# Kernel optimization log

Measured on AMD Instinct MI355X. Metric: run time of the kernel, lower is better.

## Reference

```python
import jax, jax.numpy as jnp
import numpy as np

DIM = 512
HEADS = 8
DIM_HEAD = 64
DIM_INNER = HEADS * DIM_HEAD
NULL_KV = 2
CD_ITERS = 50
CD_K = 8.0
CD_EPS = 0.1
LN_EPS = 1e-5


def setup_inputs() -> dict:
    key = jax.random.key(0)
    k0, k1, k2, k3 = jax.random.split(key, 4)
    b, n = 1, 1024
    x = jax.random.normal(k0, (b, n, DIM), dtype=jnp.float32)
    w_qkv = jax.random.normal(k1, (DIM, 3 * DIM_INNER), dtype=jnp.float32) * (DIM ** -0.5)
    w_out = jax.random.normal(k2, (DIM_INNER, DIM), dtype=jnp.float32) * (DIM_INNER ** -0.5)
    null_kv = jax.random.normal(k3, (2, HEADS, NULL_KV, DIM_HEAD), dtype=jnp.float32)
    ln_g = jnp.ones((DIM,), dtype=jnp.float32)
    ln_b = jnp.zeros((DIM,), dtype=jnp.float32)
    return {"x": x, "w_qkv": w_qkv, "w_out": w_out, "null_kv": null_kv,
            "ln_g": ln_g, "ln_b": ln_b}


def _coor_descent(s, mask, k, n_iters, eps):
    # s: (b, h, i, j); mask True = attend. eps_decay==1 upstream => eps fixed.
    mask_value = -jnp.finfo(s.dtype).max
    logk = jnp.log(jnp.asarray(k, dtype=s.dtype))
    s = jnp.where(mask, s, mask_value)

    def step(carry, _):
        a, b = carry
        sb = jnp.where(mask, (s + b) / eps, mask_value)
        a = eps * (logk - jax.nn.logsumexp(sb, axis=-1, keepdims=True))
        b = -jax.nn.relu(-s - a)
        return (a, b), None

    a0 = jnp.zeros(s.shape[:-1] + (1,), dtype=s.dtype)
    b0 = -s
    (a, b), _ = jax.lax.scan(jax.checkpoint(step), (a0, b0), None, length=n_iters)
    scores = jnp.exp((s + a + b) / eps)
    return jnp.where(mask, scores, 0.0)


def reference(x, w_qkv, w_out, null_kv, ln_g, ln_b):
    b, n, _ = x.shape
    # LayerNorm (biased variance, torch default eps)
    mu = jnp.mean(x, axis=-1, keepdims=True)
    var = jnp.var(x, axis=-1, keepdims=True)
    xn = (x - mu) / jnp.sqrt(var + LN_EPS) * ln_g + ln_b

    qkv = xn @ w_qkv                                  # (b, n, 3*dim_inner)
    q, k, v = jnp.split(qkv, 3, axis=-1)
    to_heads = lambda t: t.reshape(b, n, HEADS, DIM_HEAD).transpose(0, 2, 1, 3)
    q, k, v = to_heads(q), to_heads(k), to_heads(v)   # (b, h, n, d)

    nk = jnp.broadcast_to(null_kv[0], (b, HEADS, NULL_KV, DIM_HEAD))
    nv = jnp.broadcast_to(null_kv[1], (b, HEADS, NULL_KV, DIM_HEAD))
    k = jnp.concatenate([nk, k], axis=-2)             # (b, h, n+nkv, d)
    v = jnp.concatenate([nv, v], axis=-2)

    q = q * (DIM_HEAD ** -0.5)
    sim = jnp.einsum('bhid,bhjd->bhij', q, k)         # (b, h, i, j)
    i, j = sim.shape[-2:]
    causal = jnp.triu(jnp.ones((i, j), dtype=bool), j - i + 1)
    mask = ~causal                                    # True = attend (null kv always visible)

    attn = _coor_descent(sim, mask, CD_K, CD_ITERS, CD_EPS)
    out = jnp.einsum('bhij,bhjd->bhid', attn, v)
    out = out.transpose(0, 2, 1, 3).reshape(b, n, DIM_INNER)
    return out @ w_out
```

## Files before the change

### kernel.cpp

```cpp
#include <hip/hip_runtime.h>
#include <math.h>

#define NHEAD 8
#define SROW 1088
#define PBF  2176
#define VSTR 1056
#define LOGK 2.0794415416798357f

typedef __bf16 bf16x8 __attribute__((ext_vector_type(8)));
typedef __bf16 bf16x4 __attribute__((ext_vector_type(4)));
typedef float  f32x4  __attribute__((ext_vector_type(4)));

__device__ __forceinline__ void split2(float v, __bf16& hi, __bf16& lo) {
    hi = (__bf16)v; lo = (__bf16)(v - (float)hi);
}

__device__ __forceinline__ float dpp_sum64(float x) {
    int v;
    v = __builtin_amdgcn_update_dpp(0, __float_as_int(x), 0x111, 0xf, 0xf, true); x += __int_as_float(v);
    v = __builtin_amdgcn_update_dpp(0, __float_as_int(x), 0x112, 0xf, 0xf, true); x += __int_as_float(v);
    v = __builtin_amdgcn_update_dpp(0, __float_as_int(x), 0x114, 0xf, 0xf, true); x += __int_as_float(v);
    v = __builtin_amdgcn_update_dpp(0, __float_as_int(x), 0x118, 0xf, 0xf, true); x += __int_as_float(v);
    v = __builtin_amdgcn_update_dpp(0, __float_as_int(x), 0x142, 0xa, 0xf, true); x += __int_as_float(v);
    v = __builtin_amdgcn_update_dpp(0, __float_as_int(x), 0x143, 0xc, 0xf, true); x += __int_as_float(v);
    return __int_as_float(__builtin_amdgcn_readlane(__float_as_int(x), 63));
}
__device__ __forceinline__ float dpp_max64(float x) {
    int v;
    v = __builtin_amdgcn_update_dpp(__float_as_int(x), __float_as_int(x), 0x111, 0xf, 0xf, false); x = fmaxf(x, __int_as_float(v));
    v = __builtin_amdgcn_update_dpp(__float_as_int(x), __float_as_int(x), 0x112, 0xf, 0xf, false); x = fmaxf(x, __int_as_float(v));
    v = __builtin_amdgcn_update_dpp(__float_as_int(x), __float_as_int(x), 0x114, 0xf, 0xf, false); x = fmaxf(x, __int_as_float(v));
    v = __builtin_amdgcn_update_dpp(__float_as_int(x), __float_as_int(x), 0x118, 0xf, 0xf, false); x = fmaxf(x, __int_as_float(v));
    v = __builtin_amdgcn_update_dpp(__float_as_int(x), __float_as_int(x), 0x142, 0xa, 0xf, false); x = fmaxf(x, __int_as_float(v));
    v = __builtin_amdgcn_update_dpp(__float_as_int(x), __float_as_int(x), 0x143, 0xc, 0xf, false); x = fmaxf(x, __int_as_float(v));
    return __int_as_float(__builtin_amdgcn_readlane(__float_as_int(x), 63));
}

__global__ __launch_bounds__(128) void ln_split(const float* __restrict__ x,
                                                const float* __restrict__ g,
                                                const float* __restrict__ bb,
                                                __bf16* __restrict__ xnh,
                                                __bf16* __restrict__ xnl) {
    int row = blockIdx.x, tid = threadIdx.x;
    float4 v = ((const float4*)(x + row * 512))[tid];
    float s  = v.x + v.y + v.z + v.w;
    float ss = fmaf(v.x, v.x, fmaf(v.y, v.y, fmaf(v.z, v.z, v.w * v.w)));
#pragma unroll
    for (int off = 32; off; off >>= 1) {
        s  += __shfl_down(s, off);
        ss += __shfl_down(ss, off);
    }
    __shared__ float sm[4];
    if ((tid & 63) == 0) { sm[(tid >> 6) * 2] = s; sm[(tid >> 6) * 2 + 1] = ss; }
    __syncthreads();
    s = sm[0] + sm[2]; ss = sm[1] + sm[3];
    float mu   = s * (1.f / 512);
    float var  = ss * (1.f / 512) - mu * mu;
    float rstd = 1.f / sqrtf(var + 1e-5f);
    float4 gv = ((const float4*)g)[tid];
    float4 bv = ((const float4*)bb)[tid];
    float o[4];
    o[0] = (v.x - mu) * rstd * gv.x + bv.x;
    o[1] = (v.y - mu) * rstd * gv.y + bv.y;
    o[2] = (v.z - mu) * rstd * gv.z + bv.z;
    o[3] = (v.w - mu) * rstd * gv.w + bv.w;
    bf16x4 h4, l4;
#pragma unroll
    for (int e = 0; e < 4; ++e) { __bf16 hi, lo; split2(o[e], hi, lo); h4[e] = hi; l4[e] = lo; }
    *(bf16x4*)(xnh + (size_t)row * 512 + tid * 4) = h4;
    *(bf16x4*)(xnl + (size_t)row * 512 + tid * 4) = l4;
}

__global__ __launch_bounds__(256) void wsplit_qkv(const float* __restrict__ B,
                                                  __bf16* __restrict__ bh,
                                                  __bf16* __restrict__ bl) {
    __shared__ float T[64][65];
    int k0 = blockIdx.x * 64, n0 = blockIdx.y * 64, tid = threadIdx.x;
    int r = tid >> 2, c0 = (tid & 3) << 4;
#pragma unroll
    for (int u = 0; u < 4; ++u) {
        float4 w = *(const float4*)(B + (size_t)(k0 + r) * 1536 + n0 + c0 + 4 * u);
        T[r][c0 + 4 * u + 0] = w.x; T[r][c0 + 4 * u + 1] = w.y;
        T[r][c0 + 4 * u + 2] = w.z; T[r][c0 + 4 * u + 3] = w.w;
    }
    __syncthreads();
    int nr = tid >> 2, kc0 = (tid & 3) << 4;
#pragma unroll
    for (int u = 0; u < 4; ++u) {
        bf16x4 h4, l4;
#pragma unroll
        for (int e = 0; e < 4; ++e) {
            __bf16 hi, lo; split2(T[kc0 + 4 * u + e][nr], hi, lo);
            h4[e] = hi; l4[e] = lo;
        }
        *(bf16x4*)(bh + (size_t)(n0 + nr) * 512 + k0 + kc0 + 4 * u) = h4;
        *(bf16x4*)(bl + (size_t)(n0 + nr) * 512 + k0 + kc0 + 4 * u) = l4;
    }
}

__global__ __launch_bounds__(256) void wsplit_out(const float* __restrict__ B,
                                                  __bf16* __restrict__ wo) {
    __shared__ float T[64][65];
    int k0 = blockIdx.x * 64, n0 = blockIdx.y * 64, tid = threadIdx.x;
    int r = tid >> 2, c0 = (tid & 3) << 4;
#pragma unroll
    for (int u = 0; u < 4; ++u) {
        float4 w = *(const float4*)(B + (size_t)(k0 + r) * 512 + n0 + c0 + 4 * u);
        T[r][c0 + 4 * u + 0] = w.x; T[r][c0 + 4 * u + 1] = w.y;
        T[r][c0 + 4 * u + 2] = w.z; T[r][c0 + 4 * u + 3] = w.w;
    }
    __syncthreads();
    int nr = tid >> 2, kc0 = (tid & 3) << 4;
#pragma unroll
    for (int u = 0; u < 4; ++u) {
        bf16x4 h4;
#pragma unroll
        for (int e = 0; e < 4; ++e) h4[e] = (__bf16)T[kc0 + 4 * u + e][nr];
        *(bf16x4*)(wo + (size_t)(n0 + nr) * 512 + k0 + kc0 + 4 * u) = h4;
    }
}

__global__ __launch_bounds__(256) void nullkv2(const float* __restrict__ nkv,
                                               __bf16* __restrict__ kh,
                                               __bf16* __restrict__ kl,
                                               __bf16* __restrict__ vT) {
    int tid = blockIdx.x * 256 + threadIdx.x;
    int d = tid & 63, p = (tid >> 6) & 1, h = tid >> 7;
    float kvf = nkv[((0 * NHEAD + h) * 2 + p) * 64 + d];
    __bf16 hi, lo; split2(kvf, hi, lo);
    kh[((size_t)h * SROW + p) * 64 + d] = hi;
    kl[((size_t)h * SROW + p) * 64 + d] = lo;
    float vf = nkv[((NHEAD + h) * 2 + p) * 64 + d];
    vT[((size_t)(h * 64) + d) * VSTR + p] = (__bf16)vf;
    int base = tid * 15;
#pragma unroll
    for (int e = 0; e < 15; ++e) {
        int z = base + e;
        int jj = 1026 + (z % 30);
        int hd = z / 30;
        vT[(size_t)hd * VSTR + jj] = (__bf16)0.f;
    }
}

__global__ __launch_bounds__(256, 2) void qkv_mfma(const __bf16* __restrict__ xh,
                                                   const __bf16* __restrict__ xl,
                                                   const __bf16* __restrict__ bh,
                                                   const __bf16* __restrict__ bl,
                                                   __bf16* __restrict__ qh,
                                                   __bf16* __restrict__ ql,
                                                   __bf16* __restrict__ kh,
                                                   __bf16* __restrict__ kl,
                                                   __bf16* __restrict__ vT) {
    int tid = threadIdx.x, l = tid & 63, w = tid >> 6;
    int m0 = blockIdx.x * 32, n0 = blockIdx.y * 64;
    int ms = (w & 1) << 4, nh2 = (w >> 1) << 5;
    int arow = m0 + ms + (l & 15);
    f32x4 acc[2] = {};
    for (int ks = 0; ks < 16; ++ks) {
        int koff = ((l >> 4) << 3) + (ks << 5);
        bf16x8 ah = *(const bf16x8*)(xh + (size_t)arow * 512 + koff);
        bf16x8 al = *(const bf16x8*)(xl + (size_t)arow * 512 + koff);
#pragma unroll
        for (int ct = 0; ct < 2; ++ct) {
            int ncol = n0 + nh2 + (ct << 4) + (l & 15);
            bf16x8 bhv = *(const bf16x8*)(bh + (size_t)ncol * 512 + koff);
            bf16x8 blv = *(const bf16x8*)(bl + (size_t)ncol * 512 + koff);
            acc[ct] = __builtin_amdgcn_mfma_f32_16x16x32_bf16(ah, bhv, acc[ct], 0, 0, 0);
            acc[ct] = __builtin_amdgcn_mfma_f32_16x16x32_bf16(al, bhv, acc[ct], 0, 0, 0);
            acc[ct] = __builtin_amdgcn_mfma_f32_16x16x32_bf16(ah, blv, acc[ct], 0, 0, 0);
        }
    }
#pragma unroll
    for (int ct = 0; ct < 2; ++ct) {
        int c = n0 + nh2 + (ct << 4) + (l & 15);
#pragma unroll
        for (int r = 0; r < 4; ++r) {
            int m = m0 + ms + ((l >> 4) << 2) + r;
            float val = acc[ct][r];
            if (c < 512) {
                int h = c >> 6, d = c & 63;
                __bf16 hi, lo; split2(val * 1.25f, hi, lo);
                qh[(((size_t)(h << 10)) + m) * 64 + d] = hi;
                ql[(((size_t)(h << 10)) + m) * 64 + d] = lo;
            } else if (c < 1024) {
                int c2 = c - 512, h = c2 >> 6, d = c2 & 63;
                __bf16 hi, lo; split2(val, hi, lo);
                kh[((size_t)h * SROW + 2 + m) * 64 + d] = hi;
                kl[((size_t)h * SROW + 2 + m) * 64 + d] = lo;
            } else {
                int c2 = c - 1024, h = c2 >> 6, d = c2 & 63;
                vT[((size_t)(h * 64) + d) * VSTR + 2 + m] = (__bf16)val;
            }
        }
    }
}

__global__ __launch_bounds__(256, 2) void qk_mfma(const __bf16* __restrict__ qh,
                                                  const __bf16* __restrict__ ql,
                                                  const __bf16* __restrict__ kh,
                                                  const __bf16* __restrict__ kl,
                                                  float* __restrict__ s) {
    int b = blockIdx.x, h = blockIdx.y;
    int ti = (int)((-3.0f + sqrtf(9.0f + 8.0f * (float)b)) * 0.5f);
    while ((ti + 1) * (ti + 4) / 2 <= b) ++ti;
    while (ti * (ti + 3) / 2 > b) --ti;
    int tj = b - ti * (ti + 3) / 2;
    int i0 = ti << 6, j0 = tj << 6;

    int tid = threadIdx.x, l = tid & 63, w = tid >> 6;
    int arow = i0 + (w << 4) + (l & 15);
    const __bf16* qhb = qh + ((size_t)(h << 10) + arow) * 64;
    const __bf16* qlb = ql + ((size_t)(h << 10) + arow) * 64;
    f32x4 acc[4] = {};
#pragma unroll
    for (int ks = 0; ks < 2; ++ks) {
        int koff = ((l >> 4) << 3) + (ks << 5);
        bf16x8 ah = *(const bf16x8*)(qhb + koff);
        bf16x8 al = *(const bf16x8*)(qlb + koff);
#pragma unroll
        for (int ct = 0; ct < 4; ++ct) {
            int j = j0 + (ct << 4) + (l & 15);
            bf16x8 bhv = *(const bf16x8*)(kh + ((size_t)h * SROW + j) * 64 + koff);
            bf16x8 blv = *(const bf16x8*)(kl + ((size_t)h * SROW + j) * 64 + koff);
            acc[ct] = __builtin_amdgcn_mfma_f32_16x16x32_bf16(ah, bhv, acc[ct], 0, 0, 0);
            acc[ct] = __builtin_amdgcn_mfma_f32_16x16x32_bf16(al, bhv, acc[ct], 0, 0, 0);
            acc[ct] = __builtin_amdgcn_mfma_f32_16x16x32_bf16(ah, blv, acc[ct], 0, 0, 0);
        }
    }
#pragma unroll
    for (int ct = 0; ct < 4; ++ct) {
        int j = j0 + (ct << 4) + (l & 15);
#pragma unroll
        for (int r = 0; r < 4; ++r) {
            int i = i0 + (w << 4) + ((l >> 4) << 2) + r;
            s[((size_t)(h << 10) + i) * SROW + j] = acc[ct][r];
        }
    }
}

__global__ __launch_bounds__(64, 4) void cd_kernel(float* __restrict__ s) {
    int lane = threadIdx.x, p = blockIdx.x;
    int h = p >> 9, ip = p & 511;
    int iA = 1023 - ip, iB = ip;
    int nvA = iA + 3, nvB = iB + 3;
    float* rA = s + ((size_t)(h << 10) + iA) * SROW;
    float* rB = s + ((size_t)(h << 10) + iB) * SROW;
    int jb = lane << 2;

    float4 sA[5], sB[3];
#pragma unroll
    for (int t = 0; t < 5; ++t) {
        if (jb + (t << 8) < SROW) sA[t] = *(const float4*)(rA + jb + (t << 8));
        else { sA[t].x = sA[t].y = sA[t].z = sA[t].w = -INFINITY; }
    }
#pragma unroll
    for (int t = 0; t < 3; ++t) sB[t] = *(const float4*)(rB + jb + (t << 8));

    float mA = -INFINITY, mB = -INFINITY;
#pragma unroll
    for (int t = 0; t < 5; ++t) {
        float* sp = (float*)&sA[t];
#pragma unroll
        for (int c = 0; c < 4; ++c) {
            int j = jb + c + (t << 8);
            float v = (j < nvA) ? sp[c] : -INFINITY;
            sp[c] = v; mA = fmaxf(mA, v);
        }
    }
#pragma unroll
    for (int t = 0; t < 3; ++t) {
        float* sp = (float*)&sB[t];
#pragma unroll
        for (int c = 0; c < 4; ++c) {
            int j = jb + c + (t << 8);
            float v = (j < nvB) ? sp[c] : -INFINITY;
            sp[c] = v; mB = fmaxf(mB, v);
        }
    }
    mA = dpp_max64(mA); mB = dpp_max64(mB);

    float4 EA[5], E2A[5], EB[3], E2B[3];
#pragma unroll
    for (int t = 0; t < 5; ++t) {
        float* sp = (float*)&sA[t]; float* ep = (float*)&EA[t]; float* e2p = (float*)&E2A[t];
#pragma unroll
        for (int c = 0; c < 4; ++c) { float e = __expf(sp[c] - mA); ep[c] = e; e2p[c] = e * e; }
    }
#pragma unroll
    for (int t = 0; t < 3; ++t) {
        float* sp = (float*)&sB[t]; float* ep = (float*)&EB[t]; float* e2p = (float*)&E2B[t];
#pragma unroll
        for (int c = 0; c < 4; ++c) { float e = __expf(sp[c] - mB); ep[c] = e; e2p[c] = e * e; }
    }

    float gA = LOGK - __logf((float)nvA) + mA;
    float gB = LOGK - __logf((float)nvB) + mB;
    bool dA = false, dB = false;
#pragma unroll 1
    for (int it = 1; it < 50; ++it) {
        if (!dA) {
            float eg = __expf(fminf(gA, 80.f));
            float a0 = 0.f, a1 = 0.f, a2 = 0.f, a3 = 0.f;
#pragma unroll
            for (int t = 0; t < 5; ++t) {
                a0 += fminf(((float*)&EA[t])[0], ((float*)&E2A[t])[0] * eg);
                a1 += fminf(((float*)&EA[t])[1], ((float*)&E2A[t])[1] * eg);
                a2 += fminf(((float*)&EA[t])[2], ((float*)&E2A[t])[2] * eg);
                a3 += fminf(((float*)&EA[t])[3], ((float*)&E2A[t])[3] * eg);
            }
            float sum = dpp_sum64((a0 + a1) + (a2 + a3));
            float g2 = LOGK - __logf(sum);
            dA = (__float_as_int(g2) == __float_as_int(gA));
            gA = g2;
        }
        if (!dB) {
            float eg = __expf(fminf(gB, 80.f));
            float b0 = 0.f, b1 = 0.f, b2 = 0.f, b3 = 0.f;
#pragma unroll
            for (int t = 0; t < 3; ++t) {
                b0 += fminf(((float*)&EB[t])[0], ((float*)&E2B[t])[0] * eg);
                b1 += fminf(((float*)&EB[t])[1], ((float*)&E2B[t])[1] * eg);
                b2 += fminf(((float*)&EB[t])[2], ((float*)&E2B[t])[2] * eg);
                b3 += fminf(((float*)&EB[t])[3], ((float*)&E2B[t])[3] * eg);
            }
            float sum = dpp_sum64((b0 + b1) + (b2 + b3));
            float g2 = LOGK - __logf(sum);
            dB = (__float_as_int(g2) == __float_as_int(gB));
            gB = g2;
        }
        if (dA && dB) break;
    }

    float egA = __expf(fminf(gA, 80.f));
    float egB = __expf(fminf(gB, 80.f));
    __bf16* pA = (__bf16*)rA;
    __bf16* pB = (__bf16*)rB;
#pragma unroll
    for (int t = 0; t < 5; ++t) {
        if (jb + (t << 8) < SROW) {
            bf16x4 pv;
#pragma unroll
            for (int c = 0; c < 4; ++c) {
                float wv = ((float*)&EA[t])[c] * egA;
                pv[c] = (__bf16)(wv * fminf(1.f, wv));
            }
            *(bf16x4*)(pA + jb + (t << 8)) = pv;
        }
    }
#pragma unroll
    for (int t = 0; t < 3; ++t) {
        bf16x4 pv;
#pragma unroll
        for (int c = 0; c < 4; ++c) {
            float wv = ((float*)&EB[t])[c] * egB;
            pv[c] = (__bf16)(wv * fminf(1.f, wv));
        }
        *(bf16x4*)(pB + jb + (t << 8)) = pv;
    }
    bf16x4 z4 = {};
#pragma unroll
    for (int t = 3; t < 5; ++t) {
        if (jb + (t << 8) < SROW) *(bf16x4*)(pB + jb + (t << 8)) = z4;
    }
}

__global__ __launch_bounds__(256, 2) void pv_mfma(const float* __restrict__ s,
                                                  const __bf16* __restrict__ vT,
                                                  __bf16* __restrict__ ao) {
    int i0 = blockIdx.x << 4, h = blockIdx.y;
    int tid = threadIdx.x, l = tid & 63, w = tid >> 6;
    const __bf16* pbase = (const __bf16*)s;
    int arow = i0 + (l & 15);
    int dcol = (w << 4) + (l & 15);
    const __bf16* pr = pbase + ((size_t)(h << 10) + arow) * PBF;
    const __bf16* vr = vT + ((size_t)(h << 6) + dcol) * VSTR;
    f32x4 acc0 = {}, acc1 = {};
    int kb = (l >> 4) << 3;
#pragma unroll 4
    for (int ks = 0; ks < 32; ks += 2) {
        bf16x8 a0 = *(const bf16x8*)(pr + kb + (ks << 5));
        bf16x8 b0 = *(const bf16x8*)(vr + kb + (ks << 5));
        bf16x8 a1 = *(const bf16x8*)(pr + kb + ((ks + 1) << 5));
        bf16x8 b1 = *(const bf16x8*)(vr + kb + ((ks + 1) << 5));
        acc0 = __builtin_amdgcn_mfma_f32_16x16x32_bf16(a0, b0, acc0, 0, 0, 0);
        acc1 = __builtin_amdgcn_mfma_f32_16x16x32_bf16(a1, b1, acc1, 0, 0, 0);
    }
    {
        bf16x8 a0 = *(const bf16x8*)(pr + kb + (32 << 5));
        bf16x8 b0 = *(const bf16x8*)(vr + kb + (32 << 5));
        acc0 = __builtin_amdgcn_mfma_f32_16x16x32_bf16(a0, b0, acc0, 0, 0, 0);
    }
#pragma unroll
    for (int r = 0; r < 4; ++r) {
        int i = i0 + ((l >> 4) << 2) + r;
        ao[(size_t)i * 512 + (h << 6) + dcol] = (__bf16)(acc0[r] + acc1[r]);
    }
}

__global__ __launch_bounds__(256, 2) void out_mfma(const __bf16* __restrict__ ao,
                                                   const __bf16* __restrict__ wo,
                                                   float* __restrict__ out) {
    int m0 = blockIdx.x << 4, bn = blockIdx.y;
    int tid = threadIdx.x, l = tid & 63, w = tid >> 6;
    int arow = m0 + (l & 15);
    int ncol = (bn << 6) + (w << 4) + (l & 15);
    const __bf16* ar = ao + (size_t)arow * 512;
    const __bf16* br = wo + (size_t)ncol * 512;
    f32x4 acc0 = {}, acc1 = {};
    int kb = (l >> 4) << 3;
#pragma unroll 4
    for (int ks = 0; ks < 16; ks += 2) {
        bf16x8 a0 = *(const bf16x8*)(ar + kb + (ks << 5));
        bf16x8 b0 = *(const bf16x8*)(br + kb + (ks << 5));
        bf16x8 a1 = *(const bf16x8*)(ar + kb + ((ks + 1) << 5));
        bf16x8 b1 = *(const bf16x8*)(br + kb + ((ks + 1) << 5));
        acc0 = __builtin_amdgcn_mfma_f32_16x16x32_bf16(a0, b0, acc0, 0, 0, 0);
        acc1 = __builtin_amdgcn_mfma_f32_16x16x32_bf16(a1, b1, acc1, 0, 0, 0);
    }
#pragma unroll
    for (int r = 0; r < 4; ++r) {
        int m = m0 + ((l >> 4) << 2) + r;
        out[(size_t)m * 512 + ncol] = acc0[r] + acc1[r];
    }
}

extern "C" void kernel_launch(void* const* d_in, const int* in_sizes, int n_in,
                              void* d_out, int out_size, void* d_ws, size_t ws_size,
                              hipStream_t stream) {
    const float* x      = (const float*)d_in[0];
    const float* w_qkv  = (const float*)d_in[1];
    const float* w_out  = (const float*)d_in[2];
    const float* nullkv = (const float*)d_in[3];
    const float* ln_g   = (const float*)d_in[4];
    const float* ln_b   = (const float*)d_in[5];
    float* ws = (float*)d_ws;
    float* out = (float*)d_out;

    float* base = ws;
    __bf16* xnh = (__bf16*)(base);              base += 262144;
    __bf16* xnl = (__bf16*)(base);              base += 262144;
    __bf16* wqh = (__bf16*)(base);              base += 393216;
    __bf16* wql = (__bf16*)(base);              base += 393216;
    __bf16* qh  = (__bf16*)(base);              base += 262144;
    __bf16* ql  = (__bf16*)(base);              base += 262144;
    __bf16* kh  = (__bf16*)(base);              base += 278528;
    __bf16* kl  = (__bf16*)(base);              base += 278528;
    __bf16* vT  = (__bf16*)(base);              base += 270336;
    __bf16* wo  = (__bf16*)(base);              base += 131072;
    __bf16* ao  = (__bf16*)(base);              base += 262144;
    float*  s   = base;

    hipLaunchKernelGGL(ln_split,   dim3(1024),    dim3(128), 0, stream, x, ln_g, ln_b, xnh, xnl);
    hipLaunchKernelGGL(wsplit_qkv, dim3(8, 24),   dim3(256), 0, stream, w_qkv, wqh, wql);
    hipLaunchKernelGGL(wsplit_out, dim3(8, 8),    dim3(256), 0, stream, w_out, wo);
    hipLaunchKernelGGL(nullkv2,    dim3(4),       dim3(256), 0, stream, nullkv, kh, kl, vT);
    hipLaunchKernelGGL(qkv_mfma,   dim3(32, 24),  dim3(256), 0, stream, xnh, xnl, wqh, wql, qh, ql, kh, kl, vT);
    hipLaunchKernelGGL(qk_mfma,    dim3(152, 8),  dim3(256), 0, stream, qh, ql, kh, kl, s);
    hipLaunchKernelGGL(cd_kernel,  dim3(4096),    dim3(64),  0, stream, s);
    hipLaunchKernelGGL(pv_mfma,    dim3(64, 8),   dim3(256), 0, stream, s, vT, ao);
    hipLaunchKernelGGL(out_mfma,   dim3(64, 8),   dim3(256), 0, stream, ao, wo, out);
}
```

Baseline: 180.7 us.

## Fuse prep kernels into one launch and slim coordinate-descent register footprint

Merges the layernorm split, both weight split/transposes and the null-kv setup into a single prep kernel dispatched by block index, replacing four launches with one. The coordinate-descent kernel stops keeping a separate squared-exponential array and computes e*min(1,e*eg) on the fly, which cuts register use so the launch bounds can target two waves per block and higher occupancy. This costs an extra multiply per element in the inner loop and adds branch divergence between block roles in the prep kernel.

```diff
diff --git a/kernel.cpp b/kernel.cpp
--- a/kernel.cpp
+++ b/kernel.cpp
@@ -36,109 +36,113 @@
     return __int_as_float(__builtin_amdgcn_readlane(__float_as_int(x), 63));
 }
 
-__global__ __launch_bounds__(128) void ln_split(const float* __restrict__ x,
-                                                const float* __restrict__ g,
-                                                const float* __restrict__ bb,
-                                                __bf16* __restrict__ xnh,
-                                                __bf16* __restrict__ xnl) {
-    int row = blockIdx.x, tid = threadIdx.x;
-    float4 v = ((const float4*)(x + row * 512))[tid];
-    float s  = v.x + v.y + v.z + v.w;
-    float ss = fmaf(v.x, v.x, fmaf(v.y, v.y, fmaf(v.z, v.z, v.w * v.w)));
-#pragma unroll
-    for (int off = 32; off; off >>= 1) {
-        s  += __shfl_down(s, off);
-        ss += __shfl_down(ss, off);
-    }
-    __shared__ float sm[4];
-    if ((tid & 63) == 0) { sm[(tid >> 6) * 2] = s; sm[(tid >> 6) * 2 + 1] = ss; }
-    __syncthreads();
-    s = sm[0] + sm[2]; ss = sm[1] + sm[3];
-    float mu   = s * (1.f / 512);
-    float var  = ss * (1.f / 512) - mu * mu;
-    float rstd = 1.f / sqrtf(var + 1e-5f);
-    float4 gv = ((const float4*)g)[tid];
-    float4 bv = ((const float4*)bb)[tid];
-    float o[4];
-    o[0] = (v.x - mu) * rstd * gv.x + bv.x;
-    o[1] = (v.y - mu) * rstd * gv.y + bv.y;
-    o[2] = (v.z - mu) * rstd * gv.z + bv.z;
-    o[3] = (v.w - mu) * rstd * gv.w + bv.w;
-    bf16x4 h4, l4;
-#pragma unroll
-    for (int e = 0; e < 4; ++e) { __bf16 hi, lo; split2(o[e], hi, lo); h4[e] = hi; l4[e] = lo; }
-    *(bf16x4*)(xnh + (size_t)row * 512 + tid * 4) = h4;
-    *(bf16x4*)(xnl + (size_t)row * 512 + tid * 4) = l4;
-}
-
-__global__ __launch_bounds__(256) void wsplit_qkv(const float* __restrict__ B,
-                                                  __bf16* __restrict__ bh,
-                                                  __bf16* __restrict__ bl) {
+__global__ __launch_bounds__(256) void prep_kernel(const float* __restrict__ x,
+                                                   const float* __restrict__ g,
+                                                   const float* __restrict__ bb,
+                                                   const float* __restrict__ w_qkv,
+                                                   const float* __restrict__ w_out,
+                                                   const float* __restrict__ nkv,
+                                                   __bf16* __restrict__ xnh,
+                                                   __bf16* __restrict__ xnl,
+                                                   __bf16* __restrict__ wqh,
+                                                   __bf16* __restrict__ wql,
+                                                   __bf16* __restrict__ wo,
+                                                   __bf16* __restrict__ kh,
+                                                   __bf16* __restrict__ kl,
+                                                   __bf16* __restrict__ vT) {
     __shared__ float T[64][65];
-    int k0 = blockIdx.x * 64, n0 = blockIdx.y * 64, tid = threadIdx.x;
-    int r = tid >> 2, c0 = (tid & 3) << 4;
-#pragma unroll
-    for (int u = 0; u < 4; ++u) {
-        float4 w = *(const float4*)(B + (size_t)(k0 + r) * 1536 + n0 + c0 + 4 * u);
-        T[r][c0 + 4 * u + 0] = w.x; T[r][c0 + 4 * u + 1] = w.y;
-        T[r][c0 + 4 * u + 2] = w.z; T[r][c0 + 4 * u + 3] = w.w;
-    }
-    __syncthreads();
-    int nr = tid >> 2, kc0 = (tid & 3) << 4;
-#pragma unroll
-    for (int u = 0; u < 4; ++u) {
+    __shared__ float sm[2][4];
+    int b = blockIdx.x, tid = threadIdx.x;
+
+    if (b < 512) {
+        int half = tid >> 7, t = tid & 127;
+        int row = (b << 1) + half;
+        float4 v = ((const float4*)(x + (size_t)row * 512))[t];
+        float s  = v.x + v.y + v.z + v.w;
+        float ss = fmaf(v.x, v.x, fmaf(v.y, v.y, fmaf(v.z, v.z, v.w * v.w)));
+#pragma unroll
+        for (int off = 32; off; off >>= 1) {
+            s  += __shfl_down(s, off);
+            ss += __shfl_down(ss, off);
+        }
+        int wih = (tid >> 6) & 1;
+        if ((tid & 63) == 0) { sm[half][wih * 2] = s; sm[half][wih * 2 + 1] = ss; }
+        __syncthreads();
+        s = sm[half][0] + sm[half][2]; ss = sm[half][1] + sm[half][3];
+        float mu   = s * (1.f / 512);
+        float var  = ss * (1.f / 512) - mu * mu;
+        float rstd = 1.f / sqrtf(var + 1e-5f);
+        float4 gv = ((const float4*)g)[t];
+        float4 bv = ((const float4*)bb)[t];
+        float o[4];
+        o[0] = (v.x - mu) * rstd * gv.x + bv.x;
+        o[1] = (v.y - mu) * rstd * gv.y + bv.y;
+        o[2] = (v.z - mu) * rstd * gv.z + bv.z;
+        o[3] = (v.w - mu) * rstd * gv.w + bv.w;
         bf16x4 h4, l4;
 #pragma unroll
-        for (int e = 0; e < 4; ++e) {
-            __bf16 hi, lo; split2(T[kc0 + 4 * u + e][nr], hi, lo);
-            h4[e] = hi; l4[e] = lo;
-        }
-        *(bf16x4*)(bh + (size_t)(n0 + nr) * 512 + k0 + kc0 + 4 * u) = h4;
-        *(bf16x4*)(bl + (size_t)(n0 + nr) * 512 + k0 + kc0 + 4 * u) = l4;
-    }
-}
-
-__global__ __launch_bounds__(256) void wsplit_out(const float* __restrict__ B,
-                                                  __bf16* __restrict__ wo) {
-    __shared__ float T[64][65];
-    int k0 = blockIdx.x * 64, n0 = blockIdx.y * 64, tid = threadIdx.x;
-    int r = tid >> 2, c0 = (tid & 3) << 4;
-#pragma unroll
-    for (int u = 0; u < 4; ++u) {
-        float4 w = *(const float4*)(B + (size_t)(k0 + r) * 512 + n0 + c0 + 4 * u);
-        T[r][c0 + 4 * u + 0] = w.x; T[r][c0 + 4 * u + 1] = w.y;
-        T[r][c0 + 4 * u + 2] = w.z; T[r][c0 + 4 * u + 3] = w.w;
-    }
-    __syncthreads();
-    int nr = tid >> 2, kc0 = (tid & 3) << 4;
-#pragma unroll
-    for (int u = 0; u < 4; ++u) {
-        bf16x4 h4;
-#pragma unroll
-        for (int e = 0; e < 4; ++e) h4[e] = (__bf16)T[kc0 + 4 * u + e][nr];
-        *(bf16x4*)(wo + (size_t)(n0 + nr) * 512 + k0 + kc0 + 4 * u) = h4;
-    }
-}
-
-__global__ __launch_bounds__(256) void nullkv2(const float* __restrict__ nkv,
-                                               __bf16* __restrict__ kh,
-                                               __bf16* __restrict__ kl,
-                                               __bf16* __restrict__ vT) {
-    int tid = blockIdx.x * 256 + threadIdx.x;
-    int d = tid & 63, p = (tid >> 6) & 1, h = tid >> 7;
-    float kvf = nkv[((0 * NHEAD + h) * 2 + p) * 64 + d];
-    __bf16 hi, lo; split2(kvf, hi, lo);
-    kh[((size_t)h * SROW + p) * 64 + d] = hi;
-    kl[((size_t)h * SROW + p) * 64 + d] = lo;
-    float vf = nkv[((NHEAD + h) * 2 + p) * 64 + d];
-    vT[((size_t)(h * 64) + d) * VSTR + p] = (__bf16)vf;
-    int base = tid * 15;
-#pragma unroll
-    for (int e = 0; e < 15; ++e) {
-        int z = base + e;
-        int jj = 1026 + (z % 30);
-        int hd = z / 30;
-        vT[(size_t)hd * VSTR + jj] = (__bf16)0.f;
+        for (int e = 0; e < 4; ++e) { __bf16 hi, lo; split2(o[e], hi, lo); h4[e] = hi; l4[e] = lo; }
+        *(bf16x4*)(xnh + (size_t)row * 512 + t * 4) = h4;
+        *(bf16x4*)(xnl + (size_t)row * 512 + t * 4) = l4;
+    } else if (b < 704) {
+        int b2 = b - 512;
+        int k0 = (b2 & 7) * 64, n0 = (b2 >> 3) * 64;
+        int r = tid >> 2, c0 = (tid & 3) << 4;
+#pragma unroll
+        for (int u = 0; u < 4; ++u) {
+            float4 w = *(const float4*)(w_qkv + (size_t)(k0 + r) * 1536 + n0 + c0 + 4 * u);
+            T[r][c0 + 4 * u + 0] = w.x; T[r][c0 + 4 * u + 1] = w.y;
+            T[r][c0 + 4 * u + 2] = w.z; T[r][c0 + 4 * u + 3] = w.w;
+        }
+        __syncthreads();
+        int nr = tid >> 2, kc0 = (tid & 3) << 4;
+#pragma unroll
+        for (int u = 0; u < 4; ++u) {
+            bf16x4 h4, l4;
+#pragma unroll
+            for (int e = 0; e < 4; ++e) {
+                __bf16 hi, lo; split2(T[kc0 + 4 * u + e][nr], hi, lo);
+                h4[e] = hi; l4[e] = lo;
+            }
+            *(bf16x4*)(wqh + (size_t)(n0 + nr) * 512 + k0 + kc0 + 4 * u) = h4;
+            *(bf16x4*)(wql + (size_t)(n0 + nr) * 512 + k0 + kc0 + 4 * u) = l4;
+        }
+    } else if (b < 768) {
+        int b2 = b - 704;
+        int k0 = (b2 & 7) * 64, n0 = (b2 >> 3) * 64;
+        int r = tid >> 2, c0 = (tid & 3) << 4;
+#pragma unroll
+        for (int u = 0; u < 4; ++u) {
+            float4 w = *(const float4*)(w_out + (size_t)(k0 + r) * 512 + n0 + c0 + 4 * u);
+            T[r][c0 + 4 * u + 0] = w.x; T[r][c0 + 4 * u + 1] = w.y;
+            T[r][c0 + 4 * u + 2] = w.z; T[r][c0 + 4 * u + 3] = w.w;
+        }
+        __syncthreads();
+        int nr = tid >> 2, kc0 = (tid & 3) << 4;
+#pragma unroll
+        for (int u = 0; u < 4; ++u) {
+            bf16x4 h4;
+#pragma unroll
+            for (int e = 0; e < 4; ++e) h4[e] = (__bf16)T[kc0 + 4 * u + e][nr];
+            *(bf16x4*)(wo + (size_t)(n0 + nr) * 512 + k0 + kc0 + 4 * u) = h4;
+        }
+    } else {
+        int t2 = (b - 768) * 256 + tid;
+        int d = t2 & 63, p = (t2 >> 6) & 1, h = t2 >> 7;
+        float kvf = nkv[((0 * NHEAD + h) * 2 + p) * 64 + d];
+        __bf16 hi, lo; split2(kvf, hi, lo);
+        kh[((size_t)h * SROW + p) * 64 + d] = hi;
+        kl[((size_t)h * SROW + p) * 64 + d] = lo;
+        float vf = nkv[((NHEAD + h) * 2 + p) * 64 + d];
+        vT[((size_t)(h * 64) + d) * VSTR + p] = (__bf16)vf;
+        int base = t2 * 15;
+#pragma unroll
+        for (int e = 0; e < 15; ++e) {
+            int z = base + e;
+            int jj = 1026 + (z % 30);
+            int hd = z / 30;
+            vT[(size_t)hd * VSTR + jj] = (__bf16)0.f;
+        }
     }
 }
 
@@ -238,8 +242,9 @@
     }
 }
 
-__global__ __launch_bounds__(64, 4) void cd_kernel(float* __restrict__ s) {
-    int lane = threadIdx.x, p = blockIdx.x;
+__global__ __launch_bounds__(128, 8) void cd_kernel(float* __restrict__ s) {
+    int lane = threadIdx.x & 63;
+    int p = (blockIdx.x << 1) + (threadIdx.x >> 6);
     int h = p >> 9, ip = p & 511;
     int iA = 1023 - ip, iB = ip;
     int nvA = iA + 3, nvB = iB + 3;
@@ -247,19 +252,19 @@
     float* rB = s + ((size_t)(h << 10) + iB) * SROW;
     int jb = lane << 2;
 
-    float4 sA[5], sB[3];
+    float4 EA[5], EB[3];
 #pragma unroll
     for (int t = 0; t < 5; ++t) {
-        if (jb + (t << 8) < SROW) sA[t] = *(const float4*)(rA + jb + (t << 8));
-        else { sA[t].x = sA[t].y = sA[t].z = sA[t].w = -INFINITY; }
-    }
-#pragma unroll
-    for (int t = 0; t < 3; ++t) sB[t] = *(const float4*)(rB + jb + (t << 8));
+        if (jb + (t << 8) < SROW) EA[t] = *(const float4*)(rA + jb + (t << 8));
+        else { EA[t].x = EA[t].y = EA[t].z = EA[t].w = -INFINITY; }
+    }
+#pragma unroll
+    for (int t = 0; t < 3; ++t) EB[t] = *(const float4*)(rB + jb + (t << 8));
 
     float mA = -INFINITY, mB = -INFINITY;
 #pragma unroll
     for (int t = 0; t < 5; ++t) {
-        float* sp = (float*)&sA[t];
+        float* sp = (float*)&EA[t];
 #pragma unroll
         for (int c = 0; c < 4; ++c) {
             int j = jb + c + (t << 8);
@@ -269,7 +274,7 @@
     }
 #pragma unroll
     for (int t = 0; t < 3; ++t) {
-        float* sp = (float*)&sB[t];
+        float* sp = (float*)&EB[t];
 #pragma unroll
         for (int c = 0; c < 4; ++c) {
             int j = jb + c + (t << 8);
@@ -279,18 +284,17 @@
     }
     mA = dpp_max64(mA); mB = dpp_max64(mB);
 
-    float4 EA[5], E2A[5], EB[3], E2B[3];
 #pragma unroll
     for (int t = 0; t < 5; ++t) {
-        float* sp = (float*)&sA[t]; float* ep = (float*)&EA[t]; float* e2p = (float*)&E2A[t];
-#pragma unroll
-        for (int c = 0; c < 4; ++c) { float e = __expf(sp[c] - mA); ep[c] = e; e2p[c] = e * e; }
+        float* sp = (float*)&EA[t];
+#pragma unroll
+        for (int c = 0; c < 4; ++c) sp[c] = __expf(sp[c] - mA);
     }
 #pragma unroll
     for (int t = 0; t < 3; ++t) {
-        float* sp = (float*)&sB[t]; float* ep = (float*)&EB[t]; float* e2p = (float*)&E2B[t];
-#pragma unroll
-        for (int c = 0; c < 4; ++c) { float e = __expf(sp[c] - mB); ep[c] = e; e2p[c] = e * e; }
+        float* sp = (float*)&EB[t];
+#pragma unroll
+        for (int c = 0; c < 4; ++c) sp[c] = __expf(sp[c] - mB);
     }
 
     float gA = LOGK - __logf((float)nvA) + mA;
@@ -303,10 +307,11 @@
             float a0 = 0.f, a1 = 0.f, a2 = 0.f, a3 = 0.f;
 #pragma unroll
             for (int t = 0; t < 5; ++t) {
-                a0 += fminf(((float*)&EA[t])[0], ((float*)&E2A[t])[0] * eg);
-                a1 += fminf(((float*)&EA[t])[1], ((float*)&E2A[t])[1] * eg);
-                a2 += fminf(((float*)&EA[t])[2], ((float*)&E2A[t])[2] * eg);
-                a3 += fminf(((float*)&EA[t])[3], ((float*)&E2A[t])[3] * eg);
+                float* ep = (float*)&EA[t];
+                a0 += ep[0] * fminf(1.f, ep[0] * eg);
+                a1 += ep[1] * fminf(1.f, ep[1] * eg);
+                a2 += ep[2] * fminf(1.f, ep[2] * eg);
+                a3 += ep[3] * fminf(1.f, ep[3] * eg);
             }
             float sum = dpp_sum64((a0 + a1) + (a2 + a3));
             float g2 = LOGK - __logf(sum);
@@ -318,10 +323,11 @@
             float b0 = 0.f, b1 = 0.f, b2 = 0.f, b3 = 0.f;
 #pragma unroll
             for (int t = 0; t < 3; ++t) {
-                b0 += fminf(((float*)&EB[t])[0], ((float*)&E2B[t])[0] * eg);
-                b1 += fminf(((float*)&EB[t])[1], ((float*)&E2B[t])[1] * eg);
-                b2 += fminf(((float*)&EB[t])[2], ((float*)&E2B[t])[2] * eg);
-                b3 += fminf(((float*)&EB[t])[3], ((float*)&E2B[t])[3] * eg);
+                float* ep = (float*)&EB[t];
+                b0 += ep[0] * fminf(1.f, ep[0] * eg);
+                b1 += ep[1] * fminf(1.f, ep[1] * eg);
+                b2 += ep[2] * fminf(1.f, ep[2] * eg);
+                b3 += ep[3] * fminf(1.f, ep[3] * eg);
             }
             float sum = dpp_sum64((b0 + b1) + (b2 + b3));
             float g2 = LOGK - __logf(sum);
@@ -339,9 +345,10 @@
     for (int t = 0; t < 5; ++t) {
         if (jb + (t << 8) < SROW) {
             bf16x4 pv;
+            float* ep = (float*)&EA[t];
 #pragma unroll
             for (int c = 0; c < 4; ++c) {
-                float wv = ((float*)&EA[t])[c] * egA;
+                float wv = ep[c] * egA;
                 pv[c] = (__bf16)(wv * fminf(1.f, wv));
             }
             *(bf16x4*)(pA + jb + (t << 8)) = pv;
@@ -350,9 +357,10 @@
 #pragma unroll
     for (int t = 0; t < 3; ++t) {
         bf16x4 pv;
+        float* ep = (float*)&EB[t];
 #pragma unroll
         for (int c = 0; c < 4; ++c) {
-            float wv = ((float*)&EB[t])[c] * egB;
+            float wv = ep[c] * egB;
             pv[c] = (__bf16)(wv * fminf(1.f, wv));
         }
         *(bf16x4*)(pB + jb + (t << 8)) = pv;
@@ -450,13 +458,12 @@
     __bf16* ao  = (__bf16*)(base);              base += 262144;
     float*  s   = base;
 
-    hipLaunchKernelGGL(ln_split,   dim3(1024),    dim3(128), 0, stream, x, ln_g, ln_b, xnh, xnl);
-    hipLaunchKernelGGL(wsplit_qkv, dim3(8, 24),   dim3(256), 0, stream, w_qkv, wqh, wql);
-    hipLaunchKernelGGL(wsplit_out, dim3(8, 8),    dim3(256), 0, stream, w_out, wo);
-    hipLaunchKernelGGL(nullkv2,    dim3(4),       dim3(256), 0, stream, nullkv, kh, kl, vT);
+    hipLaunchKernelGGL(prep_kernel, dim3(772),    dim3(256), 0, stream,
+                       x, ln_g, ln_b, w_qkv, w_out, nullkv,
+                       xnh, xnl, wqh, wql, wo, kh, kl, vT);
     hipLaunchKernelGGL(qkv_mfma,   dim3(32, 24),  dim3(256), 0, stream, xnh, xnl, wqh, wql, qh, ql, kh, kl, vT);
     hipLaunchKernelGGL(qk_mfma,    dim3(152, 8),  dim3(256), 0, stream, qh, ql, kh, kl, s);
-    hipLaunchKernelGGL(cd_kernel,  dim3(4096),    dim3(64),  0, stream, s);
+    hipLaunchKernelGGL(cd_kernel,  dim3(2048),    dim3(128), 0, stream, s);
     hipLaunchKernelGGL(pv_mfma,    dim3(64, 8),   dim3(256), 0, stream, s, vT, ao);
     hipLaunchKernelGGL(out_mfma,   dim3(64, 8),   dim3(256), 0, stream, ao, wo, out);
 }
```

Result: faster. 170.4 us (-5.7%).
